# Optimization experiments

Measured on AMD Instinct MI355X. Metric: run time of the kernel, lower is better.

The kernel has to match this reference:

```python
import jax, jax.numpy as jnp
import numpy as np

CH = 512
CK = CH // 8  # 64

def conv1x1(w, x):
    # w: [out, in], x: [B, in, H, W] -> [B, out, H, W]
    return jnp.einsum('oc,bchw->bohw', w, x)

def maxpool2(x):
    B, C, H, W = x.shape
    return x.reshape(B, C, H // 2, 2, W // 2, 2).max(axis=(3, 5))

def setup_inputs() -> dict:
    key = jax.random.key(0)
    ks = jax.random.split(key, 5)
    B, H, W = 16, 64, 64
    x = jax.random.normal(ks[0], (B, CH, H, W), dtype=jnp.float32)
    scale = 1.0 / np.sqrt(CH)
    Wt = jax.random.normal(ks[1], (CK, CH), dtype=jnp.float32) * scale
    Wp = jax.random.normal(ks[2], (CK, CH), dtype=jnp.float32) * scale
    Wg = jax.random.normal(ks[3], (CK, CH), dtype=jnp.float32) * scale
    Wo = jax.random.normal(ks[4], (CH, CK), dtype=jnp.float32) * (1.0 / np.sqrt(CK))
    gamma = jnp.float32(0.1)  # nonzero so backward through attention path is exercised
    return {'x': x, 'Wt': Wt, 'Wp': Wp, 'Wg': Wg, 'Wo': Wo, 'gamma': gamma}

def reference(x, Wt, Wp, Wg, Wo, gamma):
    B, C, H, W = x.shape
    N = H * W          # query positions
    M = N // 4         # pooled key/value positions
    theta = conv1x1(Wt, x).reshape(B, CK, N)            # [B, ck, N]
    phi = maxpool2(conv1x1(Wp, x)).reshape(B, CK, M)    # [B, ck, M]
    g = maxpool2(conv1x1(Wg, x)).reshape(B, CK, M)      # [B, ck, M]
    scores = jnp.einsum('bcn,bcm->bnm', theta, phi)     # [B, N, M]
    beta = jax.nn.softmax(scores, axis=-1)
    o = jnp.einsum('bcm,bnm->bcn', g, beta)             # [B, ck, N]
    o = conv1x1(Wo, o.reshape(B, CK, H, W))             # [B, C, H, W]
    return gamma * o + x
```

## Files before the change

kernel.cpp:

```cpp
#include <hip/hip_runtime.h>

#define CHN 512
#define CKD 64
#define NPOS 4096
#define MPOS 1024

typedef __attribute__((ext_vector_type(8))) short bf16x8;
typedef __attribute__((ext_vector_type(4))) float f32x4;
typedef __attribute__((ext_vector_type(8))) unsigned short u16x8;

static constexpr size_t OFF_O   = 0;
static constexpr size_t OFF_THT = 4194304;
static constexpr size_t OFF_PHT = 6291456;
static constexpr size_t OFF_GB  = 6815744;
static constexpr size_t OFF_WBF = 7340032;
static constexpr size_t OFF_WOB = 7389184;

__device__ __forceinline__ unsigned short f2bf(float f) {
  union { float f; unsigned int u; } v; v.f = f;
  unsigned int r = v.u + 0x7FFFu + ((v.u >> 16) & 1u);
  return (unsigned short)(r >> 16);
}

__device__ __forceinline__ void gl2lds16(const void* g, void* l) {
  __builtin_amdgcn_global_load_lds(
      (const __attribute__((address_space(1))) unsigned int*)g,
      (__attribute__((address_space(3))) unsigned int*)l, 16, 0, 0);
}

__global__ __launch_bounds__(256) void prep_w_kernel(
    const float* __restrict__ Wt, const float* __restrict__ Wp,
    const float* __restrict__ Wg, const float* __restrict__ Wo,
    unsigned short* __restrict__ wbf, unsigned short* __restrict__ wobf)
{
  int id = blockIdx.x * 256 + threadIdx.x;
  if (id < 98304) {
    int mat = id >> 15, r = id & 32767;
    const float* W = (mat == 0) ? Wt : (mat == 1) ? Wp : Wg;
    wbf[id] = f2bf(W[r]);
  } else {
    int j = id - 98304;
    wobf[j] = f2bf(Wo[j]);
  }
}

__global__ __launch_bounds__(256) void qkv_fused_kernel(
    const float* __restrict__ x,
    const unsigned short* __restrict__ wbf,
    unsigned short* __restrict__ thT, unsigned short* __restrict__ phT,
    unsigned short* __restrict__ gbf)
{
  __shared__ unsigned short sXb[64 * 132];
  __shared__ unsigned short sW[3 * 64 * 64];

  const int bx = blockIdx.x;
  const int b  = blockIdx.y;
  const int t  = threadIdx.x;
  const int w   = t >> 6;
  const int l   = t & 63;
  const int l16 = l & 15;
  const int lhi = l >> 4;
  const int n0  = bx * 128;

  const float* xb = x + (size_t)b * CHN * NPOS + n0;
  const int xrow = t >> 5;
  const int xcol4 = t & 31;

  f32x4 acc[3][2][4];
#pragma unroll
  for (int m = 0; m < 3; ++m)
#pragma unroll
    for (int nf = 0; nf < 2; ++nf)
#pragma unroll
      for (int ckf = 0; ckf < 4; ++ckf) acc[m][nf][ckf] = (f32x4){0.f, 0.f, 0.f, 0.f};

  float4 xR[8];
#pragma unroll
  for (int i = 0; i < 8; ++i)
    xR[i] = *(const float4*)(xb + (size_t)(i * 8 + xrow) * NPOS + xcol4 * 4);

  for (int c0 = 0; c0 < CHN; c0 += 64) {
    if (c0) __syncthreads();
#pragma unroll
    for (int mi = 0; mi < 6; ++mi) {
      int mat = mi >> 1;
      int row = ((mi & 1) * 4 + w) * 8 + (l >> 3);
      int sbyte = (l & 7) * 16;
      const char* g = (const char*)wbf +
          ((((size_t)mat * 64 + row) * CHN + c0) << 1) + (sbyte ^ ((row & 7) << 4));
      gl2lds16(g, (char*)sW + mi * 4096 + w * 1024);
    }
#pragma unroll
    for (int i = 0; i < 8; ++i) {
      ushort4 u;
      u.x = f2bf(xR[i].x); u.y = f2bf(xR[i].y);
      u.z = f2bf(xR[i].z); u.w = f2bf(xR[i].w);
      *(ushort4*)&sXb[(i * 8 + xrow) * 132 + xcol4 * 4] = u;
    }
    __syncthreads();

    if (c0 + 64 < CHN) {
#pragma unroll
      for (int i = 0; i < 8; ++i)
        xR[i] = *(const float4*)(xb + (size_t)(c0 + 64 + i * 8 + xrow) * NPOS + xcol4 * 4);
    }

#pragma unroll
    for (int ks = 0; ks < 2; ++ks) {
      const int cu = ks * 32 + lhi * 8;
      bf16x8 a[2];
#pragma unroll
      for (int nf = 0; nf < 2; ++nf) {
        const int rn = 16 * w + 64 * nf + l16;
        bf16x8 av;
#pragma unroll
        for (int e = 0; e < 8; ++e)
          av[e] = (short)sXb[(cu + e) * 132 + rn];
        a[nf] = av;
      }
#pragma unroll
      for (int m = 0; m < 3; ++m)
#pragma unroll
        for (int ckf = 0; ckf < 4; ++ckf) {
          int rw = ckf * 16 + l16;
          bf16x8 bb = *(const bf16x8*)&sW[m * 4096 + rw * 64 + (cu ^ ((rw & 7) * 8))];
          acc[m][0][ckf] = __builtin_amdgcn_mfma_f32_16x16x32_bf16(a[0], bb, acc[m][0][ckf], 0, 0, 0);
          acc[m][1][ckf] = __builtin_amdgcn_mfma_f32_16x16x32_bf16(a[1], bb, acc[m][1][ckf], 0, 0, 0);
        }
    }
  }

  unsigned short* th = thT + (size_t)b * NPOS * 64;
#pragma unroll
  for (int nf = 0; nf < 2; ++nf)
#pragma unroll
    for (int r = 0; r < 4; ++r) {
      int n = n0 + 16 * w + 64 * nf + lhi * 4 + r;
#pragma unroll
      for (int ckf = 0; ckf < 4; ++ckf)
        th[(size_t)n * 64 + ckf * 16 + l16] = f2bf(acc[0][nf][ckf][r]);
    }

  unsigned short* ph = phT + (size_t)b * MPOS * 64;
  unsigned short* gb = gbf + (size_t)b * CKD * MPOS;
#pragma unroll
  for (int pr = 0; pr < 2; ++pr) {
    int mcol = bx * 32 + 8 * w + lhi * 2 + pr;
#pragma unroll
    for (int ckf = 0; ckf < 4; ++ckf) {
      int ck = ckf * 16 + l16;
      float vp = fmaxf(fmaxf(acc[1][0][ckf][2 * pr], acc[1][0][ckf][2 * pr + 1]),
                       fmaxf(acc[1][1][ckf][2 * pr], acc[1][1][ckf][2 * pr + 1]));
      float vg = fmaxf(fmaxf(acc[2][0][ckf][2 * pr], acc[2][0][ckf][2 * pr + 1]),
                       fmaxf(acc[2][1][ckf][2 * pr], acc[2][1][ckf][2 * pr + 1]));
      ph[(size_t)mcol * 64 + ck] = f2bf(vp);
      gb[(size_t)ck * MPOS + mcol] = f2bf(vg);
    }
  }
}

__global__ __launch_bounds__(256) void attn_kernel(
    const unsigned short* __restrict__ thT,
    const unsigned short* __restrict__ phT,
    const unsigned short* __restrict__ gbf,
    unsigned short* __restrict__ obf)
{
  __shared__ unsigned short sTh[128 * 64];
  __shared__ unsigned short sP [128 * 64];
  __shared__ unsigned short sPhi[64 * 64];
  __shared__ unsigned short sG [64 * 64];

  const int qt = blockIdx.x;
  const int b  = blockIdx.y;
  const int t  = threadIdx.x;
  const int w   = t >> 6;
  const int l   = t & 63;
  const int l16 = l & 15;
  const int lhi = l >> 4;

  {
    const char* srcb = (const char*)(thT + ((size_t)b * NPOS + (size_t)qt * 128) * 64);
#pragma unroll
    for (int i = 0; i < 4; ++i) {
      int cidx = i * 256 + t;
      int row = cidx >> 3, sub = cidx & 7;
      gl2lds16(srcb + row * 128 + ((sub * 16) ^ ((row & 7) << 4)),
               (char*)sTh + (i * 256 + w * 64) * 16);
    }
  }

  f32x4 oacc[2][4];
  f32x4 lacc[2];
#pragma unroll
  for (int qf = 0; qf < 2; ++qf) {
    lacc[qf] = (f32x4){0.f, 0.f, 0.f, 0.f};
#pragma unroll
    for (int i = 0; i < 4; ++i) oacc[qf][i] = (f32x4){0.f, 0.f, 0.f, 0.f};
  }

  bf16x8 ones;
#pragma unroll
  for (int e = 0; e < 8; ++e) ones[e] = (short)0x3F80;

  const unsigned short* phb = phT + (size_t)b * MPOS * 64;
  const unsigned short* gb  = gbf + (size_t)b * CKD * MPOS;

  const int srow = t >> 3;
  const int ssub = t & 7;
  u16x8 phR[2], gR[2];
#pragma unroll
  for (int i = 0; i < 2; ++i) {
    int row = i * 32 + srow;
    phR[i] = *(const u16x8*)(phb + (size_t)row * 64 + ssub * 8);
    gR[i]  = *(const u16x8*)(gb + (size_t)row * MPOS + ssub * 8);
  }

  for (int mt = 0; mt < 16; ++mt) {
    __syncthreads();
#pragma unroll
    for (int i = 0; i < 2; ++i) {
      int row = i * 32 + srow;
      int off = row * 64 + ((ssub * 8) ^ ((row & 7) * 8));
      *(u16x8*)&sPhi[off] = phR[i];
      *(u16x8*)&sG[off]   = gR[i];
    }
    __syncthreads();

    if (mt + 1 < 16) {
#pragma unroll
      for (int i = 0; i < 2; ++i) {
        int row = i * 32 + srow;
        phR[i] = *(const u16x8*)(phb + (size_t)((mt + 1) * 64 + row) * 64 + ssub * 8);
        gR[i]  = *(const u16x8*)(gb + (size_t)row * MPOS + (mt + 1) * 64 + ssub * 8);
      }
    }

    f32x4 sacc[2][4];
#pragma unroll
    for (int qf = 0; qf < 2; ++qf)
#pragma unroll
      for (int mf = 0; mf < 4; ++mf) sacc[qf][mf] = (f32x4){0.f, 0.f, 0.f, 0.f};
#pragma unroll
    for (int qf = 0; qf < 2; ++qf)
#pragma unroll
      for (int ks = 0; ks < 2; ++ks) {
        const int q  = 32 * w + 16 * qf + l16;
        const int ob = lhi * 8 + 32 * ks;
        bf16x8 a = *(const bf16x8*)&sTh[q * 64 + (ob ^ ((q & 7) * 8))];
#pragma unroll
        for (int mf = 0; mf < 4; ++mf) {
          const int m = l16 + 16 * mf;
          bf16x8 bb = *(const bf16x8*)&sPhi[m * 64 + (ob ^ ((m & 7) * 8))];
          sacc[qf][mf] = __builtin_amdgcn_mfma_f32_16x16x32_bf16(a, bb, sacc[qf][mf], 0, 0, 0);
        }
      }

#pragma unroll
    for (int qf = 0; qf < 2; ++qf)
#pragma unroll
      for (int r = 0; r < 4; ++r) {
        const int qq = 32 * w + 16 * qf + lhi * 4 + r;
        const int swz = (qq & 7) * 8;
#pragma unroll
        for (int mf = 0; mf < 4; ++mf) {
          const int m = l16 + 16 * mf;
          sP[qq * 64 + ((m & 0x38) ^ swz) + (m & 7)] = f2bf(__expf(sacc[qf][mf][r]));
        }
      }

#pragma unroll
    for (int qf = 0; qf < 2; ++qf)
#pragma unroll
      for (int ks = 0; ks < 2; ++ks) {
        const int q  = 32 * w + 16 * qf + l16;
        const int ob = lhi * 8 + 32 * ks;
        bf16x8 a = *(const bf16x8*)&sP[q * 64 + (ob ^ ((q & 7) * 8))];
        lacc[qf] = __builtin_amdgcn_mfma_f32_16x16x32_bf16(a, ones, lacc[qf], 0, 0, 0);
#pragma unroll
        for (int ckf = 0; ckf < 4; ++ckf) {
          const int ck = l16 + 16 * ckf;
          bf16x8 bb = *(const bf16x8*)&sG[ck * 64 + (ob ^ ((ck & 7) * 8))];
          oacc[qf][ckf] = __builtin_amdgcn_mfma_f32_16x16x32_bf16(a, bb, oacc[qf][ckf], 0, 0, 0);
        }
      }
  }

  unsigned short* ob = obf + (size_t)b * NPOS * 64;
#pragma unroll
  for (int qf = 0; qf < 2; ++qf) {
    float inv[4];
#pragma unroll
    for (int r = 0; r < 4; ++r) inv[r] = 1.0f / lacc[qf][r];
#pragma unroll
    for (int r = 0; r < 4; ++r) {
      int n = qt * 128 + 32 * w + 16 * qf + lhi * 4 + r;
#pragma unroll
      for (int ckf = 0; ckf < 4; ++ckf)
        ob[(size_t)n * 64 + ckf * 16 + l16] = f2bf(oacc[qf][ckf][r] * inv[r]);
    }
  }
}

__global__ __launch_bounds__(256) void outconv_mfma_kernel(
    const float* __restrict__ x,
    const unsigned short* __restrict__ wobf,
    const unsigned short* __restrict__ obf,
    const float* __restrict__ gamma_p, float* __restrict__ outp)
{
  __shared__ unsigned short sO[256 * 64];
  __shared__ unsigned short sWo[64 * 64];

  const int nt = blockIdx.x;
  const int ct = blockIdx.y;
  const int b  = blockIdx.z;
  const int t  = threadIdx.x;
  const int w   = t >> 6;
  const int l   = t & 63;
  const int l16 = l & 15;
  const int lhi = l >> 4;

#pragma unroll
  for (int i = 0; i < 8; ++i) {
    int cidx = i * 256 + t;
    int row = cidx >> 3, sub = cidx & 7;
    const char* g = (const char*)obf +
        ((((size_t)b * NPOS + nt * 256 + row) * 64) << 1) + ((sub * 16) ^ ((row & 7) << 4));
    gl2lds16(g, (char*)sO + (i * 256 + w * 64) * 16);
  }
#pragma unroll
  for (int i = 0; i < 2; ++i) {
    int cidx = i * 256 + t;
    int row = cidx >> 3, sub = cidx & 7;
    const char* g = (const char*)wobf +
        ((((size_t)(ct * 64 + row)) * 64) << 1) + ((sub * 16) ^ ((row & 7) << 4));
    gl2lds16(g, (char*)sWo + (i * 256 + w * 64) * 16);
  }

  const float gv = *gamma_p;
  float4 xv[4][4];
#pragma unroll
  for (int nf = 0; nf < 4; ++nf) {
    const int n = nt * 256 + w * 64 + nf * 16 + lhi * 4;
#pragma unroll
    for (int cf = 0; cf < 4; ++cf) {
      const int co = ct * 64 + cf * 16 + l16;
      xv[nf][cf] = *(const float4*)(x + ((size_t)b * CHN + co) * NPOS + n);
    }
  }
  __syncthreads();

  f32x4 acc[4][4];
#pragma unroll
  for (int nf = 0; nf < 4; ++nf)
#pragma unroll
    for (int cf = 0; cf < 4; ++cf) acc[nf][cf] = (f32x4){0.f, 0.f, 0.f, 0.f};

#pragma unroll
  for (int ks = 0; ks < 2; ++ks) {
    const int cu = ks * 32 + lhi * 8;
    bf16x8 a[4];
#pragma unroll
    for (int nf = 0; nf < 4; ++nf) {
      int rn = w * 64 + nf * 16 + l16;
      a[nf] = *(const bf16x8*)&sO[rn * 64 + (cu ^ ((rn & 7) * 8))];
    }
#pragma unroll
    for (int cf = 0; cf < 4; ++cf) {
      int rw = cf * 16 + l16;
      bf16x8 bb = *(const bf16x8*)&sWo[rw * 64 + (cu ^ ((rw & 7) * 8))];
#pragma unroll
      for (int nf = 0; nf < 4; ++nf)
        acc[nf][cf] = __builtin_amdgcn_mfma_f32_16x16x32_bf16(a[nf], bb, acc[nf][cf], 0, 0, 0);
    }
  }

#pragma unroll
  for (int nf = 0; nf < 4; ++nf) {
    const int n = nt * 256 + w * 64 + nf * 16 + lhi * 4;
#pragma unroll
    for (int cf = 0; cf < 4; ++cf) {
      const int co = ct * 64 + cf * 16 + l16;
      const size_t off = ((size_t)b * CHN + co) * NPOS + n;
      f32x4 rr;
      rr[0] = fmaf(gv, acc[nf][cf][0], xv[nf][cf].x);
      rr[1] = fmaf(gv, acc[nf][cf][1], xv[nf][cf].y);
      rr[2] = fmaf(gv, acc[nf][cf][2], xv[nf][cf].z);
      rr[3] = fmaf(gv, acc[nf][cf][3], xv[nf][cf].w);
      __builtin_nontemporal_store(rr, (f32x4*)(outp + off));
    }
  }
}

extern "C" void kernel_launch(void* const* d_in, const int* in_sizes, int n_in,
                              void* d_out, int out_size, void* d_ws, size_t ws_size,
                              hipStream_t stream)
{
  const float* x     = (const float*)d_in[0];
  const float* Wt    = (const float*)d_in[1];
  const float* Wp    = (const float*)d_in[2];
  const float* Wg    = (const float*)d_in[3];
  const float* Wo    = (const float*)d_in[4];
  const float* gamma = (const float*)d_in[5];
  float* out = (float*)d_out;
  float* ws  = (float*)d_ws;

  unsigned short* obf = (unsigned short*)(ws + OFF_O);
  unsigned short* thT = (unsigned short*)(ws + OFF_THT);
  unsigned short* phT = (unsigned short*)(ws + OFF_PHT);
  unsigned short* gbf = (unsigned short*)(ws + OFF_GB);
  unsigned short* wbf = (unsigned short*)(ws + OFF_WBF);
  unsigned short* wob = (unsigned short*)(ws + OFF_WOB);

  prep_w_kernel<<<dim3(512), 256, 0, stream>>>(Wt, Wp, Wg, Wo, wbf, wob);
  qkv_fused_kernel<<<dim3(32, 16), 256, 0, stream>>>(x, wbf, thT, phT, gbf);
  attn_kernel<<<dim3(32, 16), 256, 0, stream>>>(thT, phT, gbf, obf);
  outconv_mfma_kernel<<<dim3(16, 8, 16), 256, 0, stream>>>(x, wob, obf, gamma, out);
}
```

Baseline: 124.8 us.

## Double-buffer x and weight prefetch in registers for projection GEMM

The projection kernel now keeps two register buffers of x tiles so loads run two chunks ahead, with the loop unrolled by two. Weight tiles are no longer copied global-to-LDS directly. They are loaded into registers one chunk ahead and then written to LDS. The goal is to hide global load latency behind the MFMA phase. In exchange, register pressure rises, which may lower occupancy or cause spills.

```diff
diff --git a/kernel.cpp b/kernel.cpp
--- a/kernel.cpp
+++ b/kernel.cpp
@@ -74,61 +74,91 @@
 #pragma unroll
       for (int ckf = 0; ckf < 4; ++ckf) acc[m][nf][ckf] = (f32x4){0.f, 0.f, 0.f, 0.f};
 
-  float4 xR[8];
-#pragma unroll
-  for (int i = 0; i < 8; ++i)
-    xR[i] = *(const float4*)(xb + (size_t)(i * 8 + xrow) * NPOS + xcol4 * 4);
-
-  for (int c0 = 0; c0 < CHN; c0 += 64) {
+#define LOADX(buf, c0)                                                         \
+  _Pragma("unroll")                                                            \
+  for (int i = 0; i < 8; ++i)                                                  \
+    buf[i] = *(const float4*)(xb + (size_t)((c0) + i * 8 + xrow) * NPOS + xcol4 * 4);
+
+#define WRITEX(buf)                                                            \
+  _Pragma("unroll")                                                            \
+  for (int i = 0; i < 8; ++i) {                                                \
+    ushort4 u;                                                                 \
+    u.x = f2bf(buf[i].x); u.y = f2bf(buf[i].y);                                \
+    u.z = f2bf(buf[i].z); u.w = f2bf(buf[i].w);                                \
+    *(ushort4*)&sXb[(i * 8 + xrow) * 132 + xcol4 * 4] = u;                     \
+  }
+
+#define LOADW(wR, c0)                                                          \
+  _Pragma("unroll")                                                            \
+  for (int mi = 0; mi < 6; ++mi) {                                             \
+    int row = ((mi & 1) * 4 + w) * 8 + (l >> 3);                               \
+    int sbyte = (l & 7) * 16;                                                  \
+    int mat = mi >> 1;                                                         \
+    wR[mi] = *(const u16x8*)((const char*)wbf +                                \
+        ((((size_t)mat * 64 + row) * CHN + (c0)) << 1) + (sbyte ^ ((row & 7) << 4))); \
+  }
+
+#define WRITEW(wR)                                                             \
+  _Pragma("unroll")                                                            \
+  for (int mi = 0; mi < 6; ++mi)                                               \
+    *(u16x8*)((char*)sW + mi * 4096 + w * 1024 + l * 16) = wR[mi];
+
+#define MFMA_PHASE()                                                           \
+  _Pragma("unroll")                                                            \
+  for (int ks = 0; ks < 2; ++ks) {                                             \
+    const int cu = ks * 32 + lhi * 8;                                          \
+    bf16x8 a[2];                                                               \
+    _Pragma("unroll")                                                          \
+    for (int nf = 0; nf < 2; ++nf) {                                           \
+      const int rn = 16 * w + 64 * nf + l16;                                   \
+      bf16x8 av;                                                               \
+      _Pragma("unroll")                                                        \
+      for (int e = 0; e < 8; ++e)                                              \
+        av[e] = (short)sXb[(cu + e) * 132 + rn];                               \
+      a[nf] = av;                                                              \
+    }                                                                          \
+    _Pragma("unroll")                                                          \
+    for (int m = 0; m < 3; ++m)                                                \
+      _Pragma("unroll")                                                        \
+      for (int ckf = 0; ckf < 4; ++ckf) {                                      \
+        int rw = ckf * 16 + l16;                                               \
+        bf16x8 bb = *(const bf16x8*)&sW[m * 4096 + rw * 64 + (cu ^ ((rw & 7) * 8))]; \
+        acc[m][0][ckf] = __builtin_amdgcn_mfma_f32_16x16x32_bf16(a[0], bb, acc[m][0][ckf], 0, 0, 0); \
+        acc[m][1][ckf] = __builtin_amdgcn_mfma_f32_16x16x32_bf16(a[1], bb, acc[m][1][ckf], 0, 0, 0); \
+      }                                                                        \
+  }
+
+  float4 xA[8], xB[8];
+  u16x8 wR[6];
+  LOADX(xA, 0);
+  LOADX(xB, 64);
+  LOADW(wR, 0);
+
+#pragma unroll
+  for (int cc = 0; cc < 4; ++cc) {
+    const int c0 = cc * 128;
     if (c0) __syncthreads();
-#pragma unroll
-    for (int mi = 0; mi < 6; ++mi) {
-      int mat = mi >> 1;
-      int row = ((mi & 1) * 4 + w) * 8 + (l >> 3);
-      int sbyte = (l & 7) * 16;
-      const char* g = (const char*)wbf +
-          ((((size_t)mat * 64 + row) * CHN + c0) << 1) + (sbyte ^ ((row & 7) << 4));
-      gl2lds16(g, (char*)sW + mi * 4096 + w * 1024);
-    }
-#pragma unroll
-    for (int i = 0; i < 8; ++i) {
-      ushort4 u;
-      u.x = f2bf(xR[i].x); u.y = f2bf(xR[i].y);
-      u.z = f2bf(xR[i].z); u.w = f2bf(xR[i].w);
-      *(ushort4*)&sXb[(i * 8 + xrow) * 132 + xcol4 * 4] = u;
-    }
+    WRITEX(xA);
+    WRITEW(wR);
     __syncthreads();
-
-    if (c0 + 64 < CHN) {
-#pragma unroll
-      for (int i = 0; i < 8; ++i)
-        xR[i] = *(const float4*)(xb + (size_t)(c0 + 64 + i * 8 + xrow) * NPOS + xcol4 * 4);
-    }
-
-#pragma unroll
-    for (int ks = 0; ks < 2; ++ks) {
-      const int cu = ks * 32 + lhi * 8;
-      bf16x8 a[2];
-#pragma unroll
-      for (int nf = 0; nf < 2; ++nf) {
-        const int rn = 16 * w + 64 * nf + l16;
-        bf16x8 av;
-#pragma unroll
-        for (int e = 0; e < 8; ++e)
-          av[e] = (short)sXb[(cu + e) * 132 + rn];
-        a[nf] = av;
-      }
-#pragma unroll
-      for (int m = 0; m < 3; ++m)
-#pragma unroll
-        for (int ckf = 0; ckf < 4; ++ckf) {
-          int rw = ckf * 16 + l16;
-          bf16x8 bb = *(const bf16x8*)&sW[m * 4096 + rw * 64 + (cu ^ ((rw & 7) * 8))];
-          acc[m][0][ckf] = __builtin_amdgcn_mfma_f32_16x16x32_bf16(a[0], bb, acc[m][0][ckf], 0, 0, 0);
-          acc[m][1][ckf] = __builtin_amdgcn_mfma_f32_16x16x32_bf16(a[1], bb, acc[m][1][ckf], 0, 0, 0);
-        }
-    }
-  }
+    if (c0 + 128 < CHN) LOADX(xA, c0 + 128);
+    LOADW(wR, c0 + 64);
+    MFMA_PHASE();
+
+    __syncthreads();
+    WRITEX(xB);
+    WRITEW(wR);
+    __syncthreads();
+    if (c0 + 192 < CHN) LOADX(xB, c0 + 192);
+    if (c0 + 128 < CHN) LOADW(wR, c0 + 128);
+    MFMA_PHASE();
+  }
+
+#undef LOADX
+#undef WRITEX
+#undef LOADW
+#undef WRITEW
+#undef MFMA_PHASE
 
   unsigned short* th = thT + (size_t)b * NPOS * 64;
 #pragma unroll
```

Result: faster. 121.6 us (-2.6%).
